# Performance work log

Measured on AMD Instinct MI355X. Metric: run time of the kernel, lower is better.

## Reference

```python
import jax, jax.numpy as jnp
import numpy as np

B, C, H, W = 2, 256, 64, 64
HEADS = 8
HEAD_DIM = C // HEADS  # 32
INNER = HEADS * HEAD_DIM  # 256
GROUPS = 32
EPS = 1e-5


def groupnorm(x, w, b):
    # x: [B, C, H, W]; normalize over (C//G, H, W) within each of G groups
    Bx, Cx, Hx, Wx = x.shape
    xg = x.reshape(Bx, GROUPS, -1)
    mu = xg.mean(axis=-1, keepdims=True)
    var = xg.var(axis=-1, keepdims=True)
    xn = ((xg - mu) * jax.lax.rsqrt(var + EPS)).reshape(Bx, Cx, Hx, Wx)
    return xn * w[:, None, None] + b[:, None, None]


def setup_inputs() -> dict:
    key = jax.random.key(0)
    k0, k1, k2 = jax.random.split(key, 3)
    x = jax.random.normal(k0, (B, C, H, W), dtype=jnp.float32)
    gn_weight = jnp.ones((C,), dtype=jnp.float32)
    gn_bias = jnp.zeros((C,), dtype=jnp.float32)
    # 1x1 conv weights (kernel dims squeezed): [out_ch, in_ch]
    w_qkv = jax.random.normal(k1, (3 * INNER, C), dtype=jnp.float32) * 0.02
    w_out = jax.random.normal(k2, (C, INNER), dtype=jnp.float32) * 0.02
    return {"x": x, "gn_weight": gn_weight, "gn_bias": gn_bias,
            "w_qkv": w_qkv, "w_out": w_out}


def reference(x, gn_weight, gn_bias, w_qkv, w_out):
    Bx, Cx, Hx, Wx = x.shape
    N = Hx * Wx
    scale = HEAD_DIM ** -0.5
    xn = groupnorm(x, gn_weight, gn_bias)
    # 1x1 conv == channel matmul
    qkv = jnp.einsum('oc,bchw->bohw', w_qkv, xn)  # [B, 3*INNER, H, W]
    q, k, v = jnp.split(qkv, 3, axis=1)
    # 'b (h d) x y -> b h (x y) d'
    def to_heads(t):
        return t.reshape(Bx, HEADS, HEAD_DIM, N).transpose(0, 1, 3, 2)  # bhnd
    q, k, v = to_heads(q), to_heads(k), to_heads(v)
    sim = jnp.einsum('bhid,bhjd->bhij', q, k) * scale  # [B, h, N, N]
    attn = jax.nn.softmax(sim, axis=-1)
    o = jnp.einsum('bhij,bhjd->bhid', attn, v)  # [B, h, N, d]
    # 'b h (x y) d -> b (h d) x y'
    o = o.transpose(0, 1, 3, 2).reshape(Bx, INNER, Hx, Wx)
    out = jnp.einsum('co,bohw->bchw', w_out, o)
    return x + out
```

## Files before the change

kernel.cpp:

```cpp
#include <hip/hip_runtime.h>
#include <hip/hip_bf16.h>

#define BATCH 2
#define CH 256
#define HW 4096
#define HEADS 8
#define HDIM 32
#define GROUPS 32
#define EPS 1e-5f
#define SCALE 0.17677669529663687f
#define QSCALE (0.17677669529663687f * 1.4426950408889634f)

typedef short s16x8 __attribute__((ext_vector_type(8)));
typedef float floatx4 __attribute__((ext_vector_type(4)));
typedef unsigned short ushort_t;
typedef unsigned int uint_t;

static __device__ __forceinline__ ushort_t f2bf(float f) {
    __hip_bfloat16 h = __float2bfloat16(f);
    return *reinterpret_cast<ushort_t*>(&h);
}

static __device__ __forceinline__ uint_t pk2(float lo, float hi) {
    return __builtin_amdgcn_perm(__float_as_uint(hi), __float_as_uint(lo), 0x07060302u);
}

static __device__ __forceinline__ void gload_lds16(const ushort_t* g, ushort_t* l) {
    __builtin_amdgcn_global_load_lds((const __attribute__((address_space(1))) void*)g,
                                     (__attribute__((address_space(3))) void*)l, 16, 0, 0);
}

__global__ void wcvt(const float* __restrict__ wq, const float* __restrict__ wo,
                     ushort_t* __restrict__ dst) {
    int i = blockIdx.x * 256 + threadIdx.x;
    float4 v = (i < 49152) ? ((const float4*)wq)[i] : ((const float4*)wo)[i - 49152];
    uint2 o;
    o.x = pk2(v.x, v.y);
    o.y = pk2(v.z, v.w);
    ushort_t p[4] = {f2bf(v.x), f2bf(v.y), f2bf(v.z), f2bf(v.w)};
    o.x = (uint_t)p[0] | ((uint_t)p[1] << 16);
    o.y = (uint_t)p[2] | ((uint_t)p[3] << 16);
    *(uint2*)&dst[(size_t)i * 4] = o;
}

__global__ void gn_stats(const float* __restrict__ x, float* __restrict__ stats) {
    int bg = blockIdx.x;
    const float4* xv = (const float4*)(x + (size_t)bg * 8 * HW);
    int t = threadIdx.x;
    float s = 0.f, ss = 0.f;
    for (int i = t; i < 8192; i += 256) {
        float4 v = xv[i];
        s  += v.x + v.y + v.z + v.w;
        ss += v.x*v.x + v.y*v.y + v.z*v.z + v.w*v.w;
    }
    #pragma unroll
    for (int off = 32; off; off >>= 1) {
        s  += __shfl_down(s, off);
        ss += __shfl_down(ss, off);
    }
    __shared__ float rs[4], rss[4];
    int wave = t >> 6;
    if ((t & 63) == 0) { rs[wave] = s; rss[wave] = ss; }
    __syncthreads();
    if (t == 0) {
        s  = rs[0] + rs[1] + rs[2] + rs[3];
        ss = rss[0] + rss[1] + rss[2] + rss[3];
        float mu  = s / 32768.f;
        float var = ss / 32768.f - mu * mu;
        stats[bg * 2]     = mu;
        stats[bg * 2 + 1] = rsqrtf(var + EPS);
    }
}

__global__ void norm_transpose(const float* __restrict__ x, const float* __restrict__ stats,
                               const float* __restrict__ gw, const float* __restrict__ gb,
                               ushort_t* __restrict__ xn) {
    __shared__ ushort_t tile[64][40];
    int b = blockIdx.z, c0 = blockIdx.y * 32, n0 = blockIdx.x * 64;
    int t = threadIdx.x;
    #pragma unroll
    for (int i = 0; i < 8; i++) {
        int idx = i * 256 + t;
        int c = idx >> 6, n = idx & 63;
        int cc = c0 + c;
        float mu   = stats[(b * GROUPS + (cc >> 3)) * 2];
        float rstd = stats[(b * GROUPS + (cc >> 3)) * 2 + 1];
        float v = x[((size_t)b * CH + cc) * HW + n0 + n];
        v = (v - mu) * rstd * gw[cc] + gb[cc];
        tile[n][c] = f2bf(v);
    }
    __syncthreads();
    int n = t >> 2, chk = t & 3;
    uint4 val = *(const uint4*)&tile[n][chk * 8];
    *(uint4*)(xn + ((size_t)(b * HW + n0 + n)) * CH + c0 + chk * 8) = val;
}

__global__ void qkv_gemm(const ushort_t* __restrict__ xn, const ushort_t* __restrict__ wqb,
                         ushort_t* __restrict__ qo, ushort_t* __restrict__ ko,
                         ushort_t* __restrict__ vo) {
    __shared__ ushort_t Al[64][40];
    __shared__ ushort_t Bl[64][40];
    int b = blockIdx.z;
    int n0 = blockIdx.x * 64, o0 = blockIdx.y * 64;
    int t = threadIdx.x, lane = t & 63, wave = t >> 6;
    int lr = lane & 15, lk = lane >> 4;
    floatx4 acc[4] = {};
    for (int k0 = 0; k0 < 256; k0 += 32) {
        int row = t >> 2, chk = t & 3;
        *(uint4*)&Al[row][chk * 8] =
            *(const uint4*)(xn + ((size_t)(b * HW + n0 + row)) * CH + k0 + chk * 8);
        *(uint4*)&Bl[row][chk * 8] =
            *(const uint4*)(wqb + (size_t)(o0 + row) * CH + k0 + chk * 8);
        __syncthreads();
        s16x8 af = *(const s16x8*)&Al[wave * 16 + lr][lk * 8];
        #pragma unroll
        for (int ct = 0; ct < 4; ct++) {
            s16x8 bf = *(const s16x8*)&Bl[ct * 16 + lr][lk * 8];
            acc[ct] = __builtin_amdgcn_mfma_f32_16x16x32_bf16(af, bf, acc[ct], 0, 0, 0);
        }
        __syncthreads();
    }
    #pragma unroll
    for (int ct = 0; ct < 4; ct++) {
        int o = o0 + ct * 16 + lr;
        int sel = o >> 8;
        int h = (o >> 5) & 7;
        int d = o & 31;
        int nrow0 = n0 + wave * 16 + (lk << 2);
        if (sel == 0) {
            #pragma unroll
            for (int r = 0; r < 4; r++)
                qo[(((size_t)(b * HEADS + h)) * HW + nrow0 + r) * HDIM + d] =
                    f2bf(acc[ct][r] * QSCALE);
        } else if (sel == 1) {
            #pragma unroll
            for (int r = 0; r < 4; r++) {
                int tt = (nrow0 + r) & 63;
                int sg = 4 * ((tt >> 3) & 3) + 16 * ((((tt >> 2) & 1) << 1) | ((tt >> 5) & 1)) + (tt & 3);
                ko[(((size_t)(b * HEADS + h)) * HW + n0 + sg) * HDIM + d] = f2bf(acc[ct][r]);
            }
        } else {
            ushort_t pk[4];
            #pragma unroll
            for (int r = 0; r < 4; r++) pk[r] = f2bf(acc[ct][r]);
            *(uint2*)&vo[(((size_t)(b * HEADS + h)) * HDIM + d) * HW + nrow0] = *(uint2*)pk;
        }
    }
}

__global__ void __launch_bounds__(256, 4)
attn5(const ushort_t* __restrict__ qg, const ushort_t* __restrict__ kg,
      const ushort_t* __restrict__ vg, ushort_t* __restrict__ og) {
    __shared__ ushort_t Kl[4][2048];
    __shared__ ushort_t Vl[4][2048];
    const int bh = blockIdx.y;
    const int n0 = blockIdx.x * 64;
    const int t = threadIdx.x;
    const int lane = t & 63, w = t >> 6;
    const int lr = lane & 15, lk = lane >> 4;

    const ushort_t* kb = kg + (size_t)bh * HW * HDIM;
    const ushort_t* vb = vg + (size_t)bh * HDIM * HW;

    const int lrr = t & 15, lkk = (t >> 4) & 3, wv = t >> 6;
    const ushort_t* gk = kb + ((wv << 4) + lrr) * HDIM + lkk * 8;
    const ushort_t* gv = vb + (size_t)(((t >> 7) << 4) + lrr) * HW + ((t >> 6) & 1) * 32 + lkk * 8;
    ushort_t* kd0 = &Kl[0][wv << 9]; ushort_t* kd1 = &Kl[1][wv << 9];
    ushort_t* kd2 = &Kl[2][wv << 9]; ushort_t* kd3 = &Kl[3][wv << 9];
    ushort_t* vd0 = &Vl[0][wv << 9]; ushort_t* vd1 = &Vl[1][wv << 9];
    ushort_t* vd2 = &Vl[2][wv << 9]; ushort_t* vd3 = &Vl[3][wv << 9];

    s16x8 qf = *(const s16x8*)(qg + ((size_t)bh * HW + n0 + w * 16 + lr) * HDIM + lk * 8);

    const s16x8 onesf = {0x3F80, 0x3F80, 0x3F80, 0x3F80, 0x3F80, 0x3F80, 0x3F80, 0x3F80};
    const floatx4 zf = {};
    floatx4 oacc[2] = {};
    floatx4 Lacc = {};

    auto step = [&](const ushort_t* Kb, const ushort_t* Vb,
                    ushort_t* kdn, ushort_t* vdn, bool dostage) {
        if (dostage) {
            gload_lds16(gk, kdn);
            gload_lds16(gv, vdn);
            gk += 64 * HDIM; gv += 64;
        }
        floatx4 sim[4];
        __builtin_amdgcn_s_setprio(1);
#pragma unroll
        for (int ct = 0; ct < 4; ct++) {
            s16x8 kf = *(const s16x8*)(Kb + ct * 512 + lane * 8);
            sim[ct] = __builtin_amdgcn_mfma_f32_16x16x32_bf16(kf, qf, zf, 0, 0, 0);
        }
        __builtin_amdgcn_s_setprio(0);
        s16x8 vf[4];
#pragma unroll
        for (int i = 0; i < 4; i++)
            vf[i] = *(const s16x8*)(Vb + i * 512 + lane * 8);
        float p[4][4];
#pragma unroll
        for (int ct = 0; ct < 4; ct++)
#pragma unroll
            for (int r = 0; r < 4; r++) p[ct][r] = __builtin_amdgcn_exp2f(sim[ct][r]);
        s16x8 pf[2];
#pragma unroll
        for (int s = 0; s < 2; s++) {
            union { uint_t u[4]; s16x8 v; } pu;
            pu.u[0] = pk2(p[s][0], p[s][1]);
            pu.u[1] = pk2(p[s][2], p[s][3]);
            pu.u[2] = pk2(p[s + 2][0], p[s + 2][1]);
            pu.u[3] = pk2(p[s + 2][2], p[s + 2][3]);
            pf[s] = pu.v;
        }
        __builtin_amdgcn_s_setprio(1);
#pragma unroll
        for (int s = 0; s < 2; s++) {
            oacc[0] = __builtin_amdgcn_mfma_f32_16x16x32_bf16(vf[s],     pf[s], oacc[0], 0, 0, 0);
            oacc[1] = __builtin_amdgcn_mfma_f32_16x16x32_bf16(vf[2 + s], pf[s], oacc[1], 0, 0, 0);
            Lacc    = __builtin_amdgcn_mfma_f32_16x16x32_bf16(onesf,     pf[s], Lacc,    0, 0, 0);
        }
        __builtin_amdgcn_s_setprio(0);
    };

#define W2 { asm volatile("s_waitcnt vmcnt(2)" ::: "memory"); __syncthreads(); }
#define W0 { asm volatile("s_waitcnt vmcnt(0)" ::: "memory"); __syncthreads(); }

    gload_lds16(gk, kd0); gload_lds16(gv, vd0); gk += 64 * HDIM; gv += 64;
    gload_lds16(gk, kd1); gload_lds16(gv, vd1); gk += 64 * HDIM; gv += 64;
    W2

    for (int kt = 0; kt < 60; kt += 4) {
        step(Kl[0], Vl[0], kd2, vd2, true); W2
        step(Kl[1], Vl[1], kd3, vd3, true); W2
        step(Kl[2], Vl[2], kd0, vd0, true); W2
        step(Kl[3], Vl[3], kd1, vd1, true); W2
    }
    step(Kl[0], Vl[0], kd2, vd2, true); W2
    step(Kl[1], Vl[1], kd3, vd3, true); W2
    step(Kl[2], Vl[2], nullptr, nullptr, false); W0
    step(Kl[3], Vl[3], nullptr, nullptr, false);
#undef W2
#undef W0

    const int b = bh >> 3, h = bh & 7;
    float inv = 1.0f / Lacc[0];
    int n = n0 + w * 16 + lr;
#pragma unroll
    for (int ct2 = 0; ct2 < 2; ct2++) {
        uint_t lo = (uint_t)f2bf(oacc[ct2][0] * inv) | ((uint_t)f2bf(oacc[ct2][1] * inv) << 16);
        uint_t hi = (uint_t)f2bf(oacc[ct2][2] * inv) | ((uint_t)f2bf(oacc[ct2][3] * inv) << 16);
        uint2 val = {lo, hi};
        *(uint2*)(og + ((size_t)b * HW + n) * CH + h * 32 + ct2 * 16 + lk * 4) = val;
    }
}

__global__ void proj_res(const ushort_t* __restrict__ oa, const ushort_t* __restrict__ wob,
                         const float* __restrict__ x, float* __restrict__ out) {
    __shared__ ushort_t Al[64][40];
    __shared__ ushort_t Bl[64][40];
    int m0 = blockIdx.x * 64;
    int c0 = blockIdx.y * 64;
    int t = threadIdx.x, lane = t & 63, wave = t >> 6;
    int lr = lane & 15, lk = lane >> 4;
    floatx4 acc[4] = {};
    for (int k0 = 0; k0 < 256; k0 += 32) {
        int row = t >> 2, chk = t & 3;
        *(uint4*)&Al[row][chk * 8] =
            *(const uint4*)(oa + (size_t)(m0 + row) * CH + k0 + chk * 8);
        *(uint4*)&Bl[row][chk * 8] =
            *(const uint4*)(wob + (size_t)(c0 + row) * CH + k0 + chk * 8);
        __syncthreads();
        s16x8 af = *(const s16x8*)&Al[wave * 16 + lr][lk * 8];
        #pragma unroll
        for (int ct = 0; ct < 4; ct++) {
            s16x8 bf = *(const s16x8*)&Bl[ct * 16 + lr][lk * 8];
            acc[ct] = __builtin_amdgcn_mfma_f32_16x16x32_bf16(af, bf, acc[ct], 0, 0, 0);
        }
        __syncthreads();
    }
    int mrow0 = m0 + wave * 16 + (lk << 2);
    int b = mrow0 >> 12;
    int n = mrow0 & 4095;
    #pragma unroll
    for (int ct = 0; ct < 4; ct++) {
        int c = c0 + ct * 16 + lr;
        const float4 xv = *(const float4*)(x + ((size_t)(b * CH + c)) * HW + n);
        float4 ov;
        ov.x = acc[ct][0] + xv.x;
        ov.y = acc[ct][1] + xv.y;
        ov.z = acc[ct][2] + xv.z;
        ov.w = acc[ct][3] + xv.w;
        *(float4*)(out + ((size_t)(b * CH + c)) * HW + n) = ov;
    }
}

extern "C" void kernel_launch(void* const* d_in, const int* in_sizes, int n_in,
                              void* d_out, int out_size, void* d_ws, size_t ws_size,
                              hipStream_t stream) {
    const float* x    = (const float*)d_in[0];
    const float* gw   = (const float*)d_in[1];
    const float* gb   = (const float*)d_in[2];
    const float* wqkv = (const float*)d_in[3];
    const float* wout = (const float*)d_in[4];
    float* out = (float*)d_out;

    char* ws = (char*)d_ws;
    float* stats = (float*)ws;
    ushort_t* xn = (ushort_t*)(ws + 512);
    size_t per = (size_t)BATCH * HW * CH;
    ushort_t* q   = xn + per;
    ushort_t* k   = q + per;
    ushort_t* v   = k + per;
    ushort_t* oa  = v + per;
    ushort_t* wqb = oa + per;
    ushort_t* wob = wqb + 196608;

    wcvt<<<256, 256, 0, stream>>>(wqkv, wout, wqb);
    gn_stats<<<64, 256, 0, stream>>>(x, stats);
    norm_transpose<<<dim3(64, 8, 2), 256, 0, stream>>>(x, stats, gw, gb, xn);
    qkv_gemm<<<dim3(64, 12, 2), 256, 0, stream>>>(xn, wqb, q, k, v);
    attn5<<<dim3(64, 16), 256, 0, stream>>>(q, k, v, oa);
    proj_res<<<dim3(128, 4), 256, 0, stream>>>(oa, wob, x, out);
}
```

Measured before the change: 93.25 us.

## Split attention key loop across two wave groups and combine partial sums in LDS

The attention kernel moves to 512 threads per block, where two groups of four waves each process alternating 64-key tiles of the same query block. Each group keeps its own partial numerator and denominator, and these are reduced through shared memory at the end. The pipeline changes from a four-deep single-stream buffer ring to a two-deep buffer per group with full vmcnt(0) waits. The goal is more waves in flight per query block to hide latency, at the cost of a final LDS reduction, shallower prefetch, and a larger block. It also drops a redundant pack in the weight conversion kernel.

Result: slower. 98.39 us (+5.5%).

```diff
diff --git a/kernel.cpp b/kernel.cpp
--- a/kernel.cpp
+++ b/kernel.cpp
@@ -34,10 +34,8 @@
                      ushort_t* __restrict__ dst) {
     int i = blockIdx.x * 256 + threadIdx.x;
     float4 v = (i < 49152) ? ((const float4*)wq)[i] : ((const float4*)wo)[i - 49152];
+    ushort_t p[4] = {f2bf(v.x), f2bf(v.y), f2bf(v.z), f2bf(v.w)};
     uint2 o;
-    o.x = pk2(v.x, v.y);
-    o.y = pk2(v.z, v.w);
-    ushort_t p[4] = {f2bf(v.x), f2bf(v.y), f2bf(v.z), f2bf(v.w)};
     o.x = (uint_t)p[0] | ((uint_t)p[1] << 16);
     o.y = (uint_t)p[2] | ((uint_t)p[3] << 16);
     *(uint2*)&dst[(size_t)i * 4] = o;
@@ -148,42 +146,47 @@
     }
 }
 
-__global__ void __launch_bounds__(256, 4)
-attn5(const ushort_t* __restrict__ qg, const ushort_t* __restrict__ kg,
+__global__ void __launch_bounds__(512, 8)
+attn6(const ushort_t* __restrict__ qg, const ushort_t* __restrict__ kg,
       const ushort_t* __restrict__ vg, ushort_t* __restrict__ og) {
-    __shared__ ushort_t Kl[4][2048];
-    __shared__ ushort_t Vl[4][2048];
+    __shared__ ushort_t Kl[2][2][2048];
+    __shared__ ushort_t Vl[2][2][2048];
     const int bh = blockIdx.y;
     const int n0 = blockIdx.x * 64;
     const int t = threadIdx.x;
     const int lane = t & 63, w = t >> 6;
+    const int p = w >> 2;
+    const int qgp = w & 3;
     const int lr = lane & 15, lk = lane >> 4;
 
     const ushort_t* kb = kg + (size_t)bh * HW * HDIM;
     const ushort_t* vb = vg + (size_t)bh * HDIM * HW;
 
-    const int lrr = t & 15, lkk = (t >> 4) & 3, wv = t >> 6;
-    const ushort_t* gk = kb + ((wv << 4) + lrr) * HDIM + lkk * 8;
-    const ushort_t* gv = vb + (size_t)(((t >> 7) << 4) + lrr) * HW + ((t >> 6) & 1) * 32 + lkk * 8;
-    ushort_t* kd0 = &Kl[0][wv << 9]; ushort_t* kd1 = &Kl[1][wv << 9];
-    ushort_t* kd2 = &Kl[2][wv << 9]; ushort_t* kd3 = &Kl[3][wv << 9];
-    ushort_t* vd0 = &Vl[0][wv << 9]; ushort_t* vd1 = &Vl[1][wv << 9];
-    ushort_t* vd2 = &Vl[2][wv << 9]; ushort_t* vd3 = &Vl[3][wv << 9];
-
-    s16x8 qf = *(const s16x8*)(qg + ((size_t)bh * HW + n0 + w * 16 + lr) * HDIM + lk * 8);
+    const int tt = t & 255;
+    const int sh = t >> 8;
+    const int lrr = tt & 15, lkk = (tt >> 4) & 3, wv4 = tt >> 6;
+    const ushort_t* gk = kb + ((size_t)(sh * 64) + (wv4 << 4) + lrr) * HDIM + lkk * 8;
+    const ushort_t* gv = vb + (size_t)(((tt >> 7) << 4) + lrr) * HW + sh * 64 + ((tt >> 6) & 1) * 32 + lkk * 8;
+    ushort_t* kd0 = &Kl[sh][0][wv4 << 9]; ushort_t* kd1 = &Kl[sh][1][wv4 << 9];
+    ushort_t* vd0 = &Vl[sh][0][wv4 << 9]; ushort_t* vd1 = &Vl[sh][1][wv4 << 9];
+
+    const ushort_t* Kb0 = &Kl[p][0][0]; const ushort_t* Kb1 = &Kl[p][1][0];
+    const ushort_t* Vb0 = &Vl[p][0][0]; const ushort_t* Vb1 = &Vl[p][1][0];
+
+    s16x8 qf = *(const s16x8*)(qg + ((size_t)bh * HW + n0 + qgp * 16 + lr) * HDIM + lk * 8);
 
     const s16x8 onesf = {0x3F80, 0x3F80, 0x3F80, 0x3F80, 0x3F80, 0x3F80, 0x3F80, 0x3F80};
     const floatx4 zf = {};
     floatx4 oacc[2] = {};
     floatx4 Lacc = {};
 
-    auto step = [&](const ushort_t* Kb, const ushort_t* Vb,
-                    ushort_t* kdn, ushort_t* vdn, bool dostage) {
-        if (dostage) {
-            gload_lds16(gk, kdn);
-            gload_lds16(gv, vdn);
-            gk += 64 * HDIM; gv += 64;
-        }
+    auto stage = [&](ushort_t* kdn, ushort_t* vdn) {
+        gload_lds16(gk, kdn);
+        gload_lds16(gv, vdn);
+        gk += 2 * 64 * HDIM;
+        gv += 2 * 64;
+    };
+    auto compute = [&](const ushort_t* Kb, const ushort_t* Vb) {
         floatx4 sim[4];
         __builtin_amdgcn_s_setprio(1);
 #pragma unroll
@@ -196,19 +199,19 @@
 #pragma unroll
         for (int i = 0; i < 4; i++)
             vf[i] = *(const s16x8*)(Vb + i * 512 + lane * 8);
-        float p[4][4];
+        float pp[4][4];
 #pragma unroll
         for (int ct = 0; ct < 4; ct++)
 #pragma unroll
-            for (int r = 0; r < 4; r++) p[ct][r] = __builtin_amdgcn_exp2f(sim[ct][r]);
+            for (int r = 0; r < 4; r++) pp[ct][r] = __builtin_amdgcn_exp2f(sim[ct][r]);
         s16x8 pf[2];
 #pragma unroll
         for (int s = 0; s < 2; s++) {
             union { uint_t u[4]; s16x8 v; } pu;
-            pu.u[0] = pk2(p[s][0], p[s][1]);
-            pu.u[1] = pk2(p[s][2], p[s][3]);
-            pu.u[2] = pk2(p[s + 2][0], p[s + 2][1]);
-            pu.u[3] = pk2(p[s + 2][2], p[s + 2][3]);
+            pu.u[0] = pk2(pp[s][0], pp[s][1]);
+            pu.u[1] = pk2(pp[s][2], pp[s][3]);
+            pu.u[2] = pk2(pp[s + 2][0], pp[s + 2][1]);
+            pu.u[3] = pk2(pp[s + 2][2], pp[s + 2][3]);
             pf[s] = pu.v;
         }
         __builtin_amdgcn_s_setprio(1);
@@ -221,35 +224,50 @@
         __builtin_amdgcn_s_setprio(0);
     };
 
-#define W2 { asm volatile("s_waitcnt vmcnt(2)" ::: "memory"); __syncthreads(); }
-#define W0 { asm volatile("s_waitcnt vmcnt(0)" ::: "memory"); __syncthreads(); }
-
-    gload_lds16(gk, kd0); gload_lds16(gv, vd0); gk += 64 * HDIM; gv += 64;
-    gload_lds16(gk, kd1); gload_lds16(gv, vd1); gk += 64 * HDIM; gv += 64;
-    W2
-
-    for (int kt = 0; kt < 60; kt += 4) {
-        step(Kl[0], Vl[0], kd2, vd2, true); W2
-        step(Kl[1], Vl[1], kd3, vd3, true); W2
-        step(Kl[2], Vl[2], kd0, vd0, true); W2
-        step(Kl[3], Vl[3], kd1, vd1, true); W2
-    }
-    step(Kl[0], Vl[0], kd2, vd2, true); W2
-    step(Kl[1], Vl[1], kd3, vd3, true); W2
-    step(Kl[2], Vl[2], nullptr, nullptr, false); W0
-    step(Kl[3], Vl[3], nullptr, nullptr, false);
-#undef W2
-#undef W0
-
-    const int b = bh >> 3, h = bh & 7;
-    float inv = 1.0f / Lacc[0];
-    int n = n0 + w * 16 + lr;
-#pragma unroll
-    for (int ct2 = 0; ct2 < 2; ct2++) {
-        uint_t lo = (uint_t)f2bf(oacc[ct2][0] * inv) | ((uint_t)f2bf(oacc[ct2][1] * inv) << 16);
-        uint_t hi = (uint_t)f2bf(oacc[ct2][2] * inv) | ((uint_t)f2bf(oacc[ct2][3] * inv) << 16);
-        uint2 val = {lo, hi};
-        *(uint2*)(og + ((size_t)b * HW + n) * CH + h * 32 + ct2 * 16 + lk * 4) = val;
+#define WB { asm volatile("s_waitcnt vmcnt(0)" ::: "memory"); __syncthreads(); }
+
+    stage(kd0, vd0);
+    WB
+    for (int s2 = 0; s2 < 16; s2++) {
+        stage(kd1, vd1);
+        compute(Kb0, Vb0);
+        WB
+        if (s2 < 15) {
+            stage(kd0, vd0);
+            compute(Kb1, Vb1);
+            WB
+        } else {
+            compute(Kb1, Vb1);
+            __syncthreads();
+        }
+    }
+#undef WB
+
+    float* sc = (float*)&Kl[0][0][0];
+    if (w >= 4) {
+        float* dst = sc + ((size_t)((w - 4) * 64 + lane)) * 12;
+        *(floatx4*)(dst)     = oacc[0];
+        *(floatx4*)(dst + 4) = oacc[1];
+        dst[8] = Lacc[0];
+    }
+    __syncthreads();
+    if (w < 4) {
+        const float* src = sc + ((size_t)(w * 64 + lane)) * 12;
+        floatx4 o0 = *(const floatx4*)(src);
+        floatx4 o1 = *(const floatx4*)(src + 4);
+        float Lt = Lacc[0] + src[8];
+        oacc[0] += o0;
+        oacc[1] += o1;
+        const int b = bh >> 3, h = bh & 7;
+        float inv = 1.0f / Lt;
+        int n = n0 + w * 16 + lr;
+#pragma unroll
+        for (int ct2 = 0; ct2 < 2; ct2++) {
+            uint_t lo = (uint_t)f2bf(oacc[ct2][0] * inv) | ((uint_t)f2bf(oacc[ct2][1] * inv) << 16);
+            uint_t hi = (uint_t)f2bf(oacc[ct2][2] * inv) | ((uint_t)f2bf(oacc[ct2][3] * inv) << 16);
+            uint2 val = {lo, hi};
+            *(uint2*)(og + ((size_t)b * HW + n) * CH + h * 32 + ct2 * 16 + lk * 4) = val;
+        }
     }
 }
 
@@ -318,6 +336,6 @@
     gn_stats<<<64, 256, 0, stream>>>(x, stats);
     norm_transpose<<<dim3(64, 8, 2), 256, 0, stream>>>(x, stats, gw, gb, xn);
     qkv_gemm<<<dim3(64, 12, 2), 256, 0, stream>>>(xn, wqb, q, k, v);
-    attn5<<<dim3(64, 16), 256, 0, stream>>>(q, k, v, oa);
+    attn6<<<dim3(64, 16), 512, 0, stream>>>(q, k, v, oa);
     proj_res<<<dim3(128, 4), 256, 0, stream>>>(oa, wob, x, out);
 }
```
